# Kernel optimization log

Hardware: AMD Instinct MI355X
Metric: run time of the kernel (lower is better)

The kernel has to match this reference:

```python
import jax, jax.numpy as jnp
import numpy as np

B, C, L, D = 8, 32, 2048, 128
R, H = 8, 4  # num_routers, num_heads


def setup_inputs() -> dict:
    key = jax.random.key(0)
    ks = jax.random.split(key, 20)
    p = lambda k, shape: jax.random.normal(k, shape, dtype=jnp.float32) * 0.02
    inp = {
        "Z": jax.random.normal(ks[0], (B, C, L, D), dtype=jnp.float32),
        "router": p(ks[1], (R, D)),
        # router_sender projections (d_model -> d_model, torch Linear stored as x@W+b)
        "Wq1": p(ks[2], (D, D)), "bq1": jnp.zeros((D,), jnp.float32),
        "Wk1": p(ks[3], (D, D)), "bk1": jnp.zeros((D,), jnp.float32),
        "Wv1": p(ks[4], (D, D)), "bv1": jnp.zeros((D,), jnp.float32),
        "Wo1": p(ks[5], (D, D)), "bo1": jnp.zeros((D,), jnp.float32),
        # router_receiver projections
        "Wq2": p(ks[6], (D, D)), "bq2": jnp.zeros((D,), jnp.float32),
        "Wk2": p(ks[7], (D, D)), "bk2": jnp.zeros((D,), jnp.float32),
        "Wv2": p(ks[8], (D, D)), "bv2": jnp.zeros((D,), jnp.float32),
        "Wo2": p(ks[9], (D, D)), "bo2": jnp.zeros((D,), jnp.float32),
        # LayerNorm
        "gamma": jnp.ones((D,), jnp.float32),
        "beta": jnp.zeros((D,), jnp.float32),
    }
    return inp


def _cross_attn(q_in, k_in, v_in, Wq, bq, Wk, bk, Wv, bv, Wo, bo):
    # Informer FullAttention + AttentionLayer (dropout=0)
    Bn, Lq, Dm = q_in.shape
    Lk = k_in.shape[1]
    dh = Dm // H
    q = (q_in @ Wq + bq).reshape(Bn, Lq, H, dh)
    k = (k_in @ Wk + bk).reshape(Bn, Lk, H, dh)
    v = (v_in @ Wv + bv).reshape(Bn, Lk, H, dh)
    scale = 1.0 / np.sqrt(dh)
    scores = jnp.einsum("blhe,bshe->bhls", q, k) * scale
    A = jax.nn.softmax(scores, axis=-1)
    out = jnp.einsum("bhls,bshd->blhd", A, v).reshape(Bn, Lq, Dm)
    return out @ Wo + bo


def _layernorm(x, gamma, beta, eps=1e-5):
    mu = jnp.mean(x, axis=-1, keepdims=True)
    var = jnp.mean(jnp.square(x - mu), axis=-1, keepdims=True)
    return (x - mu) * jax.lax.rsqrt(var + eps) * gamma + beta


def reference(Z, router, Wq1, bq1, Wk1, bk1, Wv1, bv1, Wo1, bo1,
              Wq2, bq2, Wk2, bk2, Wv2, bv2, Wo2, bo2, gamma, beta):
    Bz, Cz, Lz, Dz = Z.shape
    x = Z.reshape(Bz * Cz, Lz, Dz)
    batch_router = jnp.broadcast_to(router[None], (Bz * Cz, R, Dz))
    # stage 1: routers attend to the sequence (R x L)
    router_buffer = _cross_attn(batch_router, x, x,
                                Wq1, bq1, Wk1, bk1, Wv1, bv1, Wo1, bo1)
    # stage 2: sequence attends to routers (L x R)
    router_receive = _cross_attn(x, router_buffer, router_buffer,
                                 Wq2, bq2, Wk2, bk2, Wv2, bv2, Wo2, bo2)
    out = _layernorm(x + router_receive, gamma, beta)
    return out.reshape(Bz, Cz, Lz, Dz)
```

## Files before the change

kernel.cpp:

```cpp
#include <hip/hip_runtime.h>

typedef float f4_t __attribute__((ext_vector_type(4)));
typedef __bf16 bf8_t __attribute__((ext_vector_type(8)));
typedef __bf16 bf4_t __attribute__((ext_vector_type(4)));

#define MFMA16(a,b,c) __builtin_amdgcn_mfma_f32_16x16x32_bf16((a),(b),(c),0,0,0)

static constexpr float kScale = 0.17677669529663687f;

__global__ __launch_bounds__(256) void k0_fold(
    const float* __restrict__ router, const float* __restrict__ Wq1,
    const float* __restrict__ bq1, const float* __restrict__ Wk1,
    const float* __restrict__ bk1, float* __restrict__ q1t,
    float* __restrict__ c1)
{
  __shared__ float q1[8][128];
  const int t = threadIdx.x;
  for (int idx = t; idx < 1024; idx += 256) {
    int r = idx >> 7, dp = idx & 127;
    float acc = bq1[dp];
    for (int e = 0; e < 128; ++e) acc += router[r*128 + e] * Wq1[e*128 + dp];
    q1[r][dp] = acc;
  }
  __syncthreads();
  for (int idx = t; idx < 4096; idx += 256) {
    int j = idx >> 7, e = idx & 127;
    int h = j >> 3, r = j & 7;
    float acc = 0.f;
    for (int d = 0; d < 32; ++d) acc += q1[r][h*32 + d] * Wk1[e*128 + h*32 + d];
    q1t[idx] = acc * kScale;
  }
  if (t < 32) {
    int h = t >> 3, r = t & 7;
    float acc = 0.f;
    for (int d = 0; d < 32; ++d) acc += q1[r][h*32 + d] * bk1[h*32 + d];
    c1[t] = acc * kScale;
  }
}

__global__ __launch_bounds__(512) void k1_stage1(
    const float* __restrict__ Z, const float* __restrict__ q1t_g,
    const float* __restrict__ c1_g, float* __restrict__ xap,
    float* __restrict__ lp)
{
  __shared__ __bf16 xb[64][136];
  __shared__ __bf16 xT[128][72];
  __shared__ __bf16 PT[32][72];
  __shared__ __bf16 q1t[32][136];
  __shared__ float lds_l[32];

  const int tid = threadIdx.x;
  const int bid = blockIdx.x;
  const float* xbase = Z + (size_t)bid * (1024 * 128);

  for (int idx = tid; idx < 4096; idx += 512)
    q1t[idx >> 7][idx & 127] = (__bf16)q1t_g[idx];
  if (tid < 32) lds_l[tid] = 0.f;

  const int lane = tid & 63;
  const int w = tid >> 6;
  const int lc = lane & 15;
  const int lg = lane >> 4;
  const int ms = w >> 2;
  const int ns = w & 3;
  float c1v[4];
#pragma unroll
  for (int r2 = 0; r2 < 4; ++r2) c1v[r2] = c1_g[ms*16 + lg*4 + r2];

  const f4_t fzero = {0.f, 0.f, 0.f, 0.f};
  f4_t accxa[2] = { fzero, fzero };
  float Lacc[4] = {0.f, 0.f, 0.f, 0.f};

  __syncthreads();

  for (int tile = 0; tile < 16; ++tile) {
    const float* xt = xbase + tile * (64 * 128);
#pragma unroll
    for (int i = 0; i < 4; ++i) {
      int f = tid + i*512;
      int pos = f >> 5, d0 = (f & 31) << 2;
      float4 v = *(const float4*)(xt + pos*128 + d0);
      bf4_t b4 = { (__bf16)v.x, (__bf16)v.y, (__bf16)v.z, (__bf16)v.w };
      *(bf4_t*)&xb[pos][d0] = b4;
    }
    __syncthreads();
#pragma unroll
    for (int s = 0; s < 2; ++s) {
      int u = tid + s*512;
      int dim = u & 127, pb = (u >> 7) << 3;
      bf8_t t8;
#pragma unroll
      for (int p = 0; p < 8; ++p) t8[p] = xb[pb + p][dim];
      *(bf8_t*)&xT[dim][pb] = t8;
    }
    f4_t sacc = fzero;
#pragma unroll
    for (int ks = 0; ks < 4; ++ks) {
      bf8_t a = *(const bf8_t*)&q1t[ms*16 + lc][ks*32 + lg*8];
      bf8_t b = *(const bf8_t*)&xb[ns*16 + lc][ks*32 + lg*8];
      sacc = MFMA16(a, b, sacc);
    }
    const int posn = ns*16 + lc;
#pragma unroll
    for (int r2 = 0; r2 < 4; ++r2) {
      float p = __expf(sacc[r2] + c1v[r2]);
      Lacc[r2] += p;
      PT[ms*16 + lg*4 + r2][posn] = (__bf16)p;
    }
    __syncthreads();
#pragma unroll
    for (int nt = 0; nt < 2; ++nt) {
      const int dimt = (ns << 1) + nt;
#pragma unroll
      for (int ks = 0; ks < 2; ++ks) {
        bf8_t a = *(const bf8_t*)&PT[ms*16 + lc][ks*32 + lg*8];
        bf8_t b = *(const bf8_t*)&xT[dimt*16 + lc][ks*32 + lg*8];
        accxa[nt] = MFMA16(a, b, accxa[nt]);
      }
    }
    __syncthreads();
  }

#pragma unroll
  for (int r2 = 0; r2 < 4; ++r2) {
    float v = Lacc[r2];
    v += __shfl_xor(v, 1);
    v += __shfl_xor(v, 2);
    v += __shfl_xor(v, 4);
    v += __shfl_xor(v, 8);
    if (lc == 0) atomicAdd(&lds_l[ms*16 + lg*4 + r2], v);
  }
  __syncthreads();

  float* xo = xap + (size_t)bid * 4096;
#pragma unroll
  for (int nt = 0; nt < 2; ++nt) {
    const int dim = ((ns << 1) + nt)*16 + lc;
#pragma unroll
    for (int r2 = 0; r2 < 4; ++r2) {
      int j = ms*16 + lg*4 + r2;
      xo[j*128 + dim] = accxa[nt][r2];
    }
  }
  if (tid < 32) lp[bid*32 + tid] = lds_l[tid];
}

__global__ __launch_bounds__(256) void k1b_mid(
    const float* __restrict__ xap, const float* __restrict__ lp,
    const float* __restrict__ Wv1, const float* __restrict__ bv1,
    const float* __restrict__ Wo1, const float* __restrict__ bo1,
    const float* __restrict__ Wk2, const float* __restrict__ bk2,
    const float* __restrict__ Wv2, const float* __restrict__ bv2,
    const float* __restrict__ Wq2, const float* __restrict__ bq2,
    const float* __restrict__ Wo2,
    float* __restrict__ kt2, float* __restrict__ c2, float* __restrict__ vt2)
{
  __shared__ float xa[32][129];
  __shared__ float invl[32];
  __shared__ float out1[8][128];
  __shared__ float rb[8][128];
  __shared__ float k2s[8][128];
  __shared__ float v2s[8][128];

  const int t = threadIdx.x, b = blockIdx.x;
  const float* p0 = xap + (size_t)(b*2) * 4096;
  const float* p1 = xap + (size_t)(b*2 + 1) * 4096;
  for (int idx = t; idx < 4096; idx += 256)
    xa[idx >> 7][idx & 127] = p0[idx] + p1[idx];
  if (t < 32) invl[t] = 1.f / (lp[b*64 + t] + lp[b*64 + 32 + t]);
  __syncthreads();

  for (int idx = t; idx < 1024; idx += 256) {
    int r = idx >> 7, hd = idx & 127, h = hd >> 5;
    int j = h*8 + r;
    float acc = 0.f;
    for (int e = 0; e < 128; ++e) acc += xa[j][e] * Wv1[e*128 + hd];
    out1[r][hd] = acc * invl[j] + bv1[hd];
  }
  __syncthreads();
  for (int idx = t; idx < 1024; idx += 256) {
    int r = idx >> 7, e2 = idx & 127;
    float acc = bo1[e2];
    for (int hd = 0; hd < 128; ++hd) acc += out1[r][hd] * Wo1[hd*128 + e2];
    rb[r][e2] = acc;
  }
  __syncthreads();
  for (int idx = t; idx < 2048; idx += 256) {
    int sel = idx >> 10;
    int r = (idx >> 7) & 7, hd = idx & 127;
    const float* W = sel ? Wv2 : Wk2;
    const float* bb = sel ? bv2 : bk2;
    float acc = bb[hd];
    for (int e = 0; e < 128; ++e) acc += rb[r][e] * W[e*128 + hd];
    float (*dst)[128] = sel ? v2s : k2s;
    dst[r][hd] = acc;
  }
  __syncthreads();
  for (int idx = t; idx < 4096; idx += 256) {
    int j = idx >> 7, e = idx & 127;
    int h = j >> 3, r = j & 7;
    float acck = 0.f, accv = 0.f;
    for (int d = 0; d < 32; ++d) {
      acck += Wq2[e*128 + h*32 + d] * k2s[r][h*32 + d];
      accv += v2s[r][h*32 + d] * Wo2[(h*32 + d)*128 + e];
    }
    kt2[(size_t)b*4096 + j*128 + e] = acck * kScale;
    vt2[(size_t)b*4096 + e*32 + j] = accv;
  }
  if (t < 32) {
    int h = t >> 3, r = t & 7;
    float acc = 0.f;
    for (int d = 0; d < 32; ++d) acc += bq2[h*32 + d] * k2s[r][h*32 + d];
    c2[b*32 + t] = acc * kScale;
  }
}

__global__ __launch_bounds__(256) void k2_stage2(
    const float* __restrict__ Z, const float* __restrict__ kt2,
    const float* __restrict__ c2g, const float* __restrict__ vt2,
    const float* __restrict__ bo2, const float* __restrict__ gamma,
    const float* __restrict__ beta, float* __restrict__ out)
{
  __shared__ __bf16 xb[64][136];
  __shared__ __bf16 kt[32][136];
  __shared__ __bf16 vT[128][56];
  __shared__ __bf16 P2[64][56];

  const int tid = threadIdx.x;
  const int bid = blockIdx.x;
  const int batch = bid >> 5;
  const size_t rowbase = (size_t)bid * (64 * 128);
  const float* x = Z + rowbase;
  float* y = out + rowbase;

  const float* ktg = kt2 + (size_t)batch * 4096;
  const float* vtg = vt2 + (size_t)batch * 4096;
  for (int idx = tid; idx < 4096; idx += 256) {
    kt[idx >> 7][idx & 127] = (__bf16)ktg[idx];
    vT[idx >> 5][idx & 31] = (__bf16)vtg[idx];
  }
#pragma unroll
  for (int i = 0; i < 8; ++i) {
    int f = tid + i*256;
    int pos = f >> 5, d0 = (f & 31) << 2;
    float4 v = *(const float4*)(x + pos*128 + d0);
    bf4_t b4 = { (__bf16)v.x, (__bf16)v.y, (__bf16)v.z, (__bf16)v.w };
    *(bf4_t*)&xb[pos][d0] = b4;
  }
  __syncthreads();

  const int lane = tid & 63;
  const int w = tid >> 6;
  const int lc = lane & 15;
  const int lg = lane >> 4;

  const f4_t fzero = {0.f, 0.f, 0.f, 0.f};

  f4_t sacc[2] = { fzero, fzero };
#pragma unroll
  for (int ks = 0; ks < 4; ++ks) {
    bf8_t a = *(const bf8_t*)&xb[w*16 + lc][ks*32 + lg*8];
#pragma unroll
    for (int nt = 0; nt < 2; ++nt) {
      bf8_t b = *(const bf8_t*)&kt[nt*16 + lc][ks*32 + lg*8];
      sacc[nt] = MFMA16(a, b, sacc[nt]);
    }
  }
  float c2v[2] = { c2g[batch*32 + lc], c2g[batch*32 + 16 + lc] };
#pragma unroll
  for (int nt = 0; nt < 2; ++nt) {
#pragma unroll
    for (int r2 = 0; r2 < 4; ++r2) {
      float s = sacc[nt][r2] + c2v[nt];
      float m = s;
      m = fmaxf(m, __shfl_xor(m, 1));
      m = fmaxf(m, __shfl_xor(m, 2));
      m = fmaxf(m, __shfl_xor(m, 4));
      float p = __expf(s - m);
      float sum = p;
      sum += __shfl_xor(sum, 1);
      sum += __shfl_xor(sum, 2);
      sum += __shfl_xor(sum, 4);
      P2[w*16 + lg*4 + r2][nt*16 + lc] = (__bf16)(p / sum);
    }
  }
  __syncthreads();

  bf8_t pa = *(const bf8_t*)&P2[w*16 + lc][lg*8];
  f4_t racc[8];
#pragma unroll
  for (int nt = 0; nt < 8; ++nt) {
    bf8_t b = *(const bf8_t*)&vT[nt*16 + lc][lg*8];
    racc[nt] = MFMA16(pa, b, fzero);
  }

  float bo2v[8], gv[8], bv[8];
#pragma unroll
  for (int nt = 0; nt < 8; ++nt) {
    int dd = nt*16 + lc;
    bo2v[nt] = bo2[dd]; gv[nt] = gamma[dd]; bv[nt] = beta[dd];
  }
#pragma unroll
  for (int r2 = 0; r2 < 4; ++r2) {
    int pos = w*16 + lg*4 + r2;
    float vv[8];
    float s1 = 0.f, s2 = 0.f;
#pragma unroll
    for (int nt = 0; nt < 8; ++nt) {
      float xv = (float)xb[pos][nt*16 + lc];
      float tv = racc[nt][r2] + bo2v[nt] + xv;
      vv[nt] = tv; s1 += tv; s2 += tv*tv;
    }
    s1 += __shfl_xor(s1, 1); s1 += __shfl_xor(s1, 2);
    s1 += __shfl_xor(s1, 4); s1 += __shfl_xor(s1, 8);
    s2 += __shfl_xor(s2, 1); s2 += __shfl_xor(s2, 2);
    s2 += __shfl_xor(s2, 4); s2 += __shfl_xor(s2, 8);
    float mean = s1 * (1.f/128.f);
    float var = s2 * (1.f/128.f) - mean*mean;
    float rstd = rsqrtf(var + 1e-5f);
#pragma unroll
    for (int nt = 0; nt < 8; ++nt)
      y[pos*128 + nt*16 + lc] = (vv[nt] - mean) * rstd * gv[nt] + bv[nt];
  }
}

extern "C" void kernel_launch(void* const* d_in, const int* in_sizes, int n_in,
                              void* d_out, int out_size, void* d_ws, size_t ws_size,
                              hipStream_t stream)
{
  const float* Z     = (const float*)d_in[0];
  const float* router= (const float*)d_in[1];
  const float* Wq1   = (const float*)d_in[2];
  const float* bq1   = (const float*)d_in[3];
  const float* Wk1   = (const float*)d_in[4];
  const float* bk1   = (const float*)d_in[5];
  const float* Wv1   = (const float*)d_in[6];
  const float* bv1   = (const float*)d_in[7];
  const float* Wo1   = (const float*)d_in[8];
  const float* bo1   = (const float*)d_in[9];
  const float* Wq2   = (const float*)d_in[10];
  const float* bq2   = (const float*)d_in[11];
  const float* Wk2   = (const float*)d_in[12];
  const float* bk2   = (const float*)d_in[13];
  const float* Wv2   = (const float*)d_in[14];
  const float* bv2   = (const float*)d_in[15];
  const float* Wo2   = (const float*)d_in[16];
  const float* bo2   = (const float*)d_in[17];
  const float* gamma = (const float*)d_in[18];
  const float* beta  = (const float*)d_in[19];
  float* out = (float*)d_out;

  float* wsf = (float*)d_ws;
  float* q1t = wsf;
  float* c1  = wsf + 4096;
  float* xap = wsf + 4352;
  float* lp  = xap + (size_t)512*4096;
  float* kt2 = lp  + 512*32;
  float* c2  = kt2 + (size_t)256*4096;
  float* vt2 = c2  + 256*32;
  (void)in_sizes; (void)n_in; (void)out_size; (void)ws_size;

  k0_fold<<<dim3(1), dim3(256), 0, stream>>>(router, Wq1, bq1, Wk1, bk1, q1t, c1);
  k1_stage1<<<dim3(512), dim3(512), 0, stream>>>(Z, q1t, c1, xap, lp);
  k1b_mid<<<dim3(256), dim3(256), 0, stream>>>(xap, lp, Wv1, bv1, Wo1, bo1,
                                               Wk2, bk2, Wv2, bv2, Wq2, bq2, Wo2,
                                               kt2, c2, vt2);
  k2_stage2<<<dim3(8192), dim3(256), 0, stream>>>(Z, kt2, c2, vt2, bo2, gamma, beta, out);
}
```

Before: 325.9 us.

## Store intermediates as bf16, double stage-2 tile, use nontemporal Z loads/stores

Stores the folded q1t, kt2 and vt2 matrices as bf16 in the workspace, so kernels copy them into shared memory with 16-byte vector loads instead of converting floats element by element. The stage-2 kernel now processes 128 rows per 512-thread block instead of 64 rows per 256 threads, which halves the per-block reload of kt/vT. Z loads in both stages and the output stores use nontemporal hints, and Z loads are batched before conversion to raise memory-level parallelism. The workspace is re-laid out by hand with byte offsets. The larger block raises shared-memory use and register pressure, and lowers the number of blocks.

```diff
diff --git a/kernel.cpp b/kernel.cpp
--- a/kernel.cpp
+++ b/kernel.cpp
@@ -11,7 +11,7 @@
 __global__ __launch_bounds__(256) void k0_fold(
     const float* __restrict__ router, const float* __restrict__ Wq1,
     const float* __restrict__ bq1, const float* __restrict__ Wk1,
-    const float* __restrict__ bk1, float* __restrict__ q1t,
+    const float* __restrict__ bk1, __bf16* __restrict__ q1t,
     float* __restrict__ c1)
 {
   __shared__ float q1[8][128];
@@ -28,7 +28,7 @@
     int h = j >> 3, r = j & 7;
     float acc = 0.f;
     for (int d = 0; d < 32; ++d) acc += q1[r][h*32 + d] * Wk1[e*128 + h*32 + d];
-    q1t[idx] = acc * kScale;
+    q1t[idx] = (__bf16)(acc * kScale);
   }
   if (t < 32) {
     int h = t >> 3, r = t & 7;
@@ -39,7 +39,7 @@
 }
 
 __global__ __launch_bounds__(512) void k1_stage1(
-    const float* __restrict__ Z, const float* __restrict__ q1t_g,
+    const float* __restrict__ Z, const __bf16* __restrict__ q1t_g,
     const float* __restrict__ c1_g, float* __restrict__ xap,
     float* __restrict__ lp)
 {
@@ -53,8 +53,10 @@
   const int bid = blockIdx.x;
   const float* xbase = Z + (size_t)bid * (1024 * 128);
 
-  for (int idx = tid; idx < 4096; idx += 512)
-    q1t[idx >> 7][idx & 127] = (__bf16)q1t_g[idx];
+  {
+    int j = tid >> 4, e0 = (tid & 15) << 3;
+    *(uint4*)&q1t[j][e0] = *(const uint4*)(q1t_g + j*128 + e0);
+  }
   if (tid < 32) lds_l[tid] = 0.f;
 
   const int lane = tid & 63;
@@ -79,7 +81,7 @@
     for (int i = 0; i < 4; ++i) {
       int f = tid + i*512;
       int pos = f >> 5, d0 = (f & 31) << 2;
-      float4 v = *(const float4*)(xt + pos*128 + d0);
+      f4_t v = __builtin_nontemporal_load((const f4_t*)(xt + pos*128 + d0));
       bf4_t b4 = { (__bf16)v.x, (__bf16)v.y, (__bf16)v.z, (__bf16)v.w };
       *(bf4_t*)&xb[pos][d0] = b4;
     }
@@ -153,7 +155,7 @@
     const float* __restrict__ Wv2, const float* __restrict__ bv2,
     const float* __restrict__ Wq2, const float* __restrict__ bq2,
     const float* __restrict__ Wo2,
-    float* __restrict__ kt2, float* __restrict__ c2, float* __restrict__ vt2)
+    __bf16* __restrict__ kt2, float* __restrict__ c2, __bf16* __restrict__ vt2)
 {
   __shared__ float xa[32][129];
   __shared__ float invl[32];
@@ -204,8 +206,8 @@
       acck += Wq2[e*128 + h*32 + d] * k2s[r][h*32 + d];
       accv += v2s[r][h*32 + d] * Wo2[(h*32 + d)*128 + e];
     }
-    kt2[(size_t)b*4096 + j*128 + e] = acck * kScale;
-    vt2[(size_t)b*4096 + e*32 + j] = accv;
+    kt2[(size_t)b*4096 + j*128 + e] = (__bf16)(acck * kScale);
+    vt2[(size_t)b*4096 + e*32 + j] = (__bf16)accv;
   }
   if (t < 32) {
     int h = t >> 3, r = t & 7;
@@ -215,36 +217,44 @@
   }
 }
 
-__global__ __launch_bounds__(256) void k2_stage2(
-    const float* __restrict__ Z, const float* __restrict__ kt2,
-    const float* __restrict__ c2g, const float* __restrict__ vt2,
+__global__ __launch_bounds__(512) void k2_stage2(
+    const float* __restrict__ Z, const __bf16* __restrict__ kt2,
+    const float* __restrict__ c2g, const __bf16* __restrict__ vt2,
     const float* __restrict__ bo2, const float* __restrict__ gamma,
     const float* __restrict__ beta, float* __restrict__ out)
 {
-  __shared__ __bf16 xb[64][136];
+  __shared__ __bf16 xb[128][136];
   __shared__ __bf16 kt[32][136];
   __shared__ __bf16 vT[128][56];
-  __shared__ __bf16 P2[64][56];
+  __shared__ __bf16 P2[128][56];
 
   const int tid = threadIdx.x;
   const int bid = blockIdx.x;
-  const int batch = bid >> 5;
-  const size_t rowbase = (size_t)bid * (64 * 128);
+  const int batch = bid >> 4;
+  const size_t rowbase = (size_t)bid * (128 * 128);
   const float* x = Z + rowbase;
   float* y = out + rowbase;
 
-  const float* ktg = kt2 + (size_t)batch * 4096;
-  const float* vtg = vt2 + (size_t)batch * 4096;
-  for (int idx = tid; idx < 4096; idx += 256) {
-    kt[idx >> 7][idx & 127] = (__bf16)ktg[idx];
-    vT[idx >> 5][idx & 31] = (__bf16)vtg[idx];
-  }
+  {
+    int j = tid >> 4, e0 = (tid & 15) << 3;
+    *(uint4*)&kt[j][e0] = *(const uint4*)(kt2 + (size_t)batch*4096 + j*128 + e0);
+  }
+  {
+    int e = tid >> 2, j0 = (tid & 3) << 3;
+    *(uint4*)&vT[e][j0] = *(const uint4*)(vt2 + (size_t)batch*4096 + e*32 + j0);
+  }
+  f4_t zv[8];
 #pragma unroll
   for (int i = 0; i < 8; ++i) {
-    int f = tid + i*256;
+    int f = tid + i*512;
     int pos = f >> 5, d0 = (f & 31) << 2;
-    float4 v = *(const float4*)(x + pos*128 + d0);
-    bf4_t b4 = { (__bf16)v.x, (__bf16)v.y, (__bf16)v.z, (__bf16)v.w };
+    zv[i] = __builtin_nontemporal_load((const f4_t*)(x + pos*128 + d0));
+  }
+#pragma unroll
+  for (int i = 0; i < 8; ++i) {
+    int f = tid + i*512;
+    int pos = f >> 5, d0 = (f & 31) << 2;
+    bf4_t b4 = { (__bf16)zv[i].x, (__bf16)zv[i].y, (__bf16)zv[i].z, (__bf16)zv[i].w };
     *(bf4_t*)&xb[pos][d0] = b4;
   }
   __syncthreads();
@@ -320,7 +330,8 @@
     float rstd = rsqrtf(var + 1e-5f);
 #pragma unroll
     for (int nt = 0; nt < 8; ++nt)
-      y[pos*128 + nt*16 + lc] = (vv[nt] - mean) * rstd * gv[nt] + bv[nt];
+      __builtin_nontemporal_store((vv[nt] - mean) * rstd * gv[nt] + bv[nt],
+                                  &y[pos*128 + nt*16 + lc]);
   }
 }
 
@@ -350,20 +361,20 @@
   const float* beta  = (const float*)d_in[19];
   float* out = (float*)d_out;
 
-  float* wsf = (float*)d_ws;
-  float* q1t = wsf;
-  float* c1  = wsf + 4096;
-  float* xap = wsf + 4352;
-  float* lp  = xap + (size_t)512*4096;
-  float* kt2 = lp  + 512*32;
-  float* c2  = kt2 + (size_t)256*4096;
-  float* vt2 = c2  + 256*32;
+  char* base = (char*)d_ws;
+  __bf16* q1tb = (__bf16*)base;
+  float*  c1   = (float*)(base + 8192);
+  float*  c2   = (float*)(base + 8448);
+  float*  lp   = (float*)(base + 41216);
+  float*  xap  = (float*)(base + 131072);
+  __bf16* kt2b = (__bf16*)(base + 131072 + 8388608);
+  __bf16* vt2b = (__bf16*)(base + 131072 + 8388608 + 2097152);
   (void)in_sizes; (void)n_in; (void)out_size; (void)ws_size;
 
-  k0_fold<<<dim3(1), dim3(256), 0, stream>>>(router, Wq1, bq1, Wk1, bk1, q1t, c1);
-  k1_stage1<<<dim3(512), dim3(512), 0, stream>>>(Z, q1t, c1, xap, lp);
+  k0_fold<<<dim3(1), dim3(256), 0, stream>>>(router, Wq1, bq1, Wk1, bk1, q1tb, c1);
+  k1_stage1<<<dim3(512), dim3(512), 0, stream>>>(Z, q1tb, c1, xap, lp);
   k1b_mid<<<dim3(256), dim3(256), 0, stream>>>(xap, lp, Wv1, bv1, Wo1, bo1,
                                                Wk2, bk2, Wv2, bv2, Wq2, bq2, Wo2,
-                                               kt2, c2, vt2);
-  k2_stage2<<<dim3(8192), dim3(256), 0, stream>>>(Z, kt2, c2, vt2, bo2, gamma, beta, out);
-}
+                                               kt2b, c2, vt2b);
+  k2_stage2<<<dim3(4096), dim3(512), 0, stream>>>(Z, kt2b, c2, vt2b, bo2, gamma, beta, out);
+}
```

After: 298.8 us. -8.3%, faster.
